# Kernel tuning notes

Hardware: AMD Instinct MI355X
Metric: run time of the kernel (lower is better)

Reference implementation:

```python
import jax, jax.numpy as jnp
import numpy as np

N = 4096
D = 512
H = 3


def setup_inputs() -> dict:
    key = jax.random.key(0)
    k1, k2, k3 = jax.random.split(key, 3)
    graph_info = (jax.random.uniform(k1, (N, N)) < 0.01).astype(jnp.float32)
    h = jax.random.normal(k2, (N, D), dtype=jnp.float32)
    # xavier_normal_ with relu gain: std = sqrt(2) * sqrt(2/(fan_in+fan_out))
    std = np.sqrt(2.0) * np.sqrt(2.0 / (D + H))
    P = jax.random.normal(k3, (D, H), dtype=jnp.float32) * jnp.float32(std)
    return {"graph_info": graph_info, "h": h, "P": P}


def reference(graph_info, h, P):
    # graph_info_1 = spmm(graph_info^T, I)^T == graph_info (identity densification)
    mask = graph_info > 0                                  # [N, N]
    E = jax.nn.relu(h @ P)                                 # [N, H] per-node scores, all heads
    NEG = jnp.float32(-9e15)
    # e is broadcast along rows: att[i, j] = E[j, k] where edge (i->j) exists
    logits = jnp.where(mask[None, :, :], E.T[:, None, :], NEG)  # [H, N, N]
    att = jax.nn.softmax(logits, axis=-1)                  # row-softmax per head
    hh = jnp.einsum('hij,jd->hid', att, h)                 # [H, N, D] aggregate
    # sum_flag == 1: scale each row i by its degree (rowsum of graph_info_1)
    rowsum = jnp.sum(graph_info, axis=-1)                  # [N]
    hh = hh * rowsum[None, :, None]
    # multi_head > 1, concat=False: sum over heads
    return jnp.sum(hh, axis=0)                             # [N, D]
```

## Files before the change

### kernel.cpp

```cpp
#include <hip/hip_runtime.h>
#include <stdint.h>

#define NN 4096
#define DD 512
#define NH 3
#define WMAX 128

typedef float        f32x4 __attribute__((ext_vector_type(4)));
typedef unsigned int u32x4 __attribute__((ext_vector_type(4)));

__device__ __forceinline__ unsigned short f2bf_rn(float x) {
    union { float f; uint32_t u; } v; v.f = x;
    uint32_t u = v.u;
    uint32_t r = (u + 0x7FFFu + ((u >> 16) & 1u)) >> 16;
    return (unsigned short)r;
}
__device__ __forceinline__ float bflo(uint32_t u) {
    union { uint32_t u; float f; } v; v.u = u << 16; return v.f;
}
__device__ __forceinline__ float bfhi(uint32_t u) {
    union { uint32_t u; float f; } v; v.u = u & 0xFFFF0000u; return v.f;
}

__global__ __launch_bounds__(256) void prep_scan_kernel(
    const float* __restrict__ g, const float* __restrict__ h,
    const float* __restrict__ P, float* __restrict__ w,
    unsigned short* __restrict__ hb, unsigned long long* __restrict__ bits)
{
    const int b = blockIdx.x;
    const int tid = threadIdx.x;
    if (b < NN) {
        const int row = b, wv = tid >> 6, ln = tid & 63;
        const f32x4* g4 = (const f32x4*)(g + (size_t)row * NN);
        f32x4 v[4];
        #pragma unroll
        for (int it = 0; it < 4; ++it)
            v[it] = __builtin_nontemporal_load(g4 + it * 256 + tid);
        #pragma unroll
        for (int it = 0; it < 4; ++it) {
            int chunk = it * 4 + wv;
            unsigned long long m0 = __ballot(v[it].x > 0.f);
            unsigned long long m1 = __ballot(v[it].y > 0.f);
            unsigned long long m2 = __ballot(v[it].z > 0.f);
            unsigned long long m3 = __ballot(v[it].w > 0.f);
            if (ln < 4) {
                unsigned long long ms = (ln == 0) ? m0 : (ln == 1) ? m1
                                       : (ln == 2) ? m2 : m3;
                bits[(size_t)row * 64 + chunk * 4 + ln] = ms;
            }
        }
        return;
    }
    int gid = (b - NN) * 256 + tid;
    int row = gid >> 6, ln = gid & 63;
    const f32x4* h4 = (const f32x4*)(h + (size_t)row * DD);
    f32x4 va = __builtin_nontemporal_load(h4 + ln * 2);
    f32x4 vb = __builtin_nontemporal_load(h4 + ln * 2 + 1);
    float e[8] = { va.x, va.y, va.z, va.w, vb.x, vb.y, vb.z, vb.w };

    u32x4 pk;
    pk.x = (uint32_t)f2bf_rn(e[0]) | ((uint32_t)f2bf_rn(e[1]) << 16);
    pk.y = (uint32_t)f2bf_rn(e[2]) | ((uint32_t)f2bf_rn(e[3]) << 16);
    pk.z = (uint32_t)f2bf_rn(e[4]) | ((uint32_t)f2bf_rn(e[5]) << 16);
    pk.w = (uint32_t)f2bf_rn(e[6]) | ((uint32_t)f2bf_rn(e[7]) << 16);
    *(u32x4*)(hb + (size_t)row * DD + ln * 8) = pk;

    int d0 = ln * 8;
    float a0 = 0.f, a1 = 0.f, a2 = 0.f;
    #pragma unroll
    for (int k = 0; k < 8; ++k) {
        float hv = e[k];
        const float* Pr = P + (size_t)(d0 + k) * NH;
        a0 = fmaf(hv, Pr[0], a0);
        a1 = fmaf(hv, Pr[1], a1);
        a2 = fmaf(hv, Pr[2], a2);
    }
    #pragma unroll
    for (int off = 32; off > 0; off >>= 1) {
        a0 += __shfl_down(a0, off);
        a1 += __shfl_down(a1, off);
        a2 += __shfl_down(a2, off);
    }
    if (ln == 0) {
        w[row * NH + 0] = expf(fmaxf(a0, 0.f));
        w[row * NH + 1] = expf(fmaxf(a1, 0.f));
        w[row * NH + 2] = expf(fmaxf(a2, 0.f));
    }
}

__global__ __launch_bounds__(256) void agg_kernel(
    const unsigned long long* __restrict__ bits,
    const unsigned short* __restrict__ hb, const float* __restrict__ w,
    float* __restrict__ out)
{
    __shared__ int s_list[4][WMAX];
    const int tid = threadIdx.x, wv = tid >> 6, ln = tid & 63;
    const int row = blockIdx.x * 4 + wv;

    unsigned long long W = bits[(size_t)row * 64 + ln];
    int cnt = __popcll(W);
    int inc = cnt;
    #pragma unroll
    for (int d = 1; d < 64; d <<= 1) {
        int n = __shfl_up(inc, d);
        if (ln >= d) inc += n;
    }
    int nnz = __shfl(inc, 63);
    int o = inc - cnt;
    int base_col = (ln >> 2) * 256 + (ln & 3);
    unsigned long long Wt = W;
    while (Wt) {
        int bp = __builtin_ctzll(Wt); Wt &= Wt - 1;
        if (o < WMAX) s_list[wv][o] = base_col + 4 * bp;
        ++o;
    }
    __syncthreads();

    float* orow = out + (size_t)row * DD + ln * 8;
    if (nnz == 0) {
        f32x4 z4 = {0.f, 0.f, 0.f, 0.f};
        *(f32x4*)(orow) = z4; *(f32x4*)(orow + 4) = z4;
        return;
    }
    int cap = nnz < WMAX ? nnz : WMAX;

    float accA[8] = {0,0,0,0,0,0,0,0};
    float accB[8] = {0,0,0,0,0,0,0,0};
    float accC[8] = {0,0,0,0,0,0,0,0};
    float z0 = 0.f, z1 = 0.f, z2 = 0.f;
    const unsigned short* hcol = hb + ln * 8;

    u32x4 r0 = {}, r1 = {};
    float wa0 = 0.f, wa1 = 0.f, wa2 = 0.f, wb0 = 0.f, wb1 = 0.f, wb2 = 0.f;
    {
        int j = s_list[wv][0];
        r0 = *(const u32x4*)(hcol + (size_t)j * DD);
        const float* wr = w + (size_t)j * NH;
        wa0 = wr[0]; wa1 = wr[1]; wa2 = wr[2];
    }
    if (cap > 1) {
        int j = s_list[wv][1];
        r1 = *(const u32x4*)(hcol + (size_t)j * DD);
        const float* wr = w + (size_t)j * NH;
        wb0 = wr[0]; wb1 = wr[1]; wb2 = wr[2];
    }
    for (int t = 0; t < cap; ++t) {
        u32x4 r = r0;
        float c0 = wa0, c1 = wa1, c2 = wa2;
        r0 = r1; wa0 = wb0; wa1 = wb1; wa2 = wb2;
        if (t + 2 < cap) {
            int j2 = s_list[wv][t + 2];
            r1 = *(const u32x4*)(hcol + (size_t)j2 * DD);
            const float* wr2 = w + (size_t)j2 * NH;
            wb0 = wr2[0]; wb1 = wr2[1]; wb2 = wr2[2];
        }
        z0 += c0; z1 += c1; z2 += c2;
        float e[8] = { bflo(r.x), bfhi(r.x), bflo(r.y), bfhi(r.y),
                       bflo(r.z), bfhi(r.z), bflo(r.w), bfhi(r.w) };
        #pragma unroll
        for (int q = 0; q < 8; ++q) {
            accA[q] = fmaf(c0, e[q], accA[q]);
            accB[q] = fmaf(c1, e[q], accB[q]);
            accC[q] = fmaf(c2, e[q], accC[q]);
        }
    }

    float rs = (float)nnz;
    float i0 = rs / z0, i1 = rs / z1, i2 = rs / z2;
    f32x4 o0, o1;
    o0.x = fmaf(accA[0], i0, fmaf(accB[0], i1, accC[0] * i2));
    o0.y = fmaf(accA[1], i0, fmaf(accB[1], i1, accC[1] * i2));
    o0.z = fmaf(accA[2], i0, fmaf(accB[2], i1, accC[2] * i2));
    o0.w = fmaf(accA[3], i0, fmaf(accB[3], i1, accC[3] * i2));
    o1.x = fmaf(accA[4], i0, fmaf(accB[4], i1, accC[4] * i2));
    o1.y = fmaf(accA[5], i0, fmaf(accB[5], i1, accC[5] * i2));
    o1.z = fmaf(accA[6], i0, fmaf(accB[6], i1, accC[6] * i2));
    o1.w = fmaf(accA[7], i0, fmaf(accB[7], i1, accC[7] * i2));
    *(f32x4*)(orow)     = o0;
    *(f32x4*)(orow + 4) = o1;
}

extern "C" void kernel_launch(void* const* d_in, const int* in_sizes, int n_in,
                              void* d_out, int out_size, void* d_ws, size_t ws_size,
                              hipStream_t stream) {
    const float* g = (const float*)d_in[0];
    const float* h = (const float*)d_in[1];
    const float* P = (const float*)d_in[2];
    float* out = (float*)d_out;

    float* w                 = (float*)d_ws;
    unsigned long long* bits = (unsigned long long*)((char*)d_ws + (64 << 10));
    unsigned short* hb       = (unsigned short*)((char*)d_ws + (64 << 10) + ((size_t)NN * 64 * 8));

    prep_scan_kernel<<<NN + (NN * 64) / 256, 256, 0, stream>>>(g, h, P, w, hb, bits);
    agg_kernel<<<NN / 4, 256, 0, stream>>>(bits, hb, w, out);
}
```

Baseline: 129.7 us.

## Fuse prep and aggregation into one cooperative kernel with grid sync

Merges the adjacency scan, bf16 conversion, score computation and aggregation into a single cooperative kernel. Each wave builds its row's neighbour list in shared memory directly via ballot/mbcnt, so the intermediate bitmask buffer and its global round trip go away. A grid-wide sync separates producing hb/w from consuming them. This removes one launch and the bits traffic, but needs all 1024 blocks co-resident, and the sync adds a barrier cost.

```diff
diff --git a/kernel.cpp b/kernel.cpp
--- a/kernel.cpp
+++ b/kernel.cpp
@@ -1,5 +1,8 @@
 #include <hip/hip_runtime.h>
+#include <hip/hip_cooperative_groups.h>
 #include <stdint.h>
+
+namespace cg = cooperative_groups;
 
 #define NN 4096
 #define DD 512
@@ -22,40 +25,17 @@
     union { uint32_t u; float f; } v; v.u = u & 0xFFFF0000u; return v.f;
 }
 
-__global__ __launch_bounds__(256) void prep_scan_kernel(
+__global__ __launch_bounds__(256, 4) void fused_att_kernel(
     const float* __restrict__ g, const float* __restrict__ h,
     const float* __restrict__ P, float* __restrict__ w,
-    unsigned short* __restrict__ hb, unsigned long long* __restrict__ bits)
+    unsigned short* __restrict__ hb, float* __restrict__ out)
 {
-    const int b = blockIdx.x;
-    const int tid = threadIdx.x;
-    if (b < NN) {
-        const int row = b, wv = tid >> 6, ln = tid & 63;
-        const f32x4* g4 = (const f32x4*)(g + (size_t)row * NN);
-        f32x4 v[4];
-        #pragma unroll
-        for (int it = 0; it < 4; ++it)
-            v[it] = __builtin_nontemporal_load(g4 + it * 256 + tid);
-        #pragma unroll
-        for (int it = 0; it < 4; ++it) {
-            int chunk = it * 4 + wv;
-            unsigned long long m0 = __ballot(v[it].x > 0.f);
-            unsigned long long m1 = __ballot(v[it].y > 0.f);
-            unsigned long long m2 = __ballot(v[it].z > 0.f);
-            unsigned long long m3 = __ballot(v[it].w > 0.f);
-            if (ln < 4) {
-                unsigned long long ms = (ln == 0) ? m0 : (ln == 1) ? m1
-                                       : (ln == 2) ? m2 : m3;
-                bits[(size_t)row * 64 + chunk * 4 + ln] = ms;
-            }
-        }
-        return;
-    }
-    int gid = (b - NN) * 256 + tid;
-    int row = gid >> 6, ln = gid & 63;
+    __shared__ int s_list[4][WMAX];
+    const int tid = threadIdx.x, wv = tid >> 6, ln = tid & 63;
+    const int row = blockIdx.x * 4 + wv;
+
     const f32x4* h4 = (const f32x4*)(h + (size_t)row * DD);
-    f32x4 va = __builtin_nontemporal_load(h4 + ln * 2);
-    f32x4 vb = __builtin_nontemporal_load(h4 + ln * 2 + 1);
+    f32x4 va = h4[ln * 2], vb = h4[ln * 2 + 1];
     float e[8] = { va.x, va.y, va.z, va.w, vb.x, vb.y, vb.z, vb.w };
 
     u32x4 pk;
@@ -65,56 +45,62 @@
     pk.w = (uint32_t)f2bf_rn(e[6]) | ((uint32_t)f2bf_rn(e[7]) << 16);
     *(u32x4*)(hb + (size_t)row * DD + ln * 8) = pk;
 
-    int d0 = ln * 8;
-    float a0 = 0.f, a1 = 0.f, a2 = 0.f;
+    {
+        int d0 = ln * 8;
+        float a0 = 0.f, a1 = 0.f, a2 = 0.f;
+        #pragma unroll
+        for (int k = 0; k < 8; ++k) {
+            float hv = e[k];
+            const float* Pr = P + (size_t)(d0 + k) * NH;
+            a0 = fmaf(hv, Pr[0], a0);
+            a1 = fmaf(hv, Pr[1], a1);
+            a2 = fmaf(hv, Pr[2], a2);
+        }
+        #pragma unroll
+        for (int off = 32; off > 0; off >>= 1) {
+            a0 += __shfl_down(a0, off);
+            a1 += __shfl_down(a1, off);
+            a2 += __shfl_down(a2, off);
+        }
+        if (ln == 0) {
+            w[row * NH + 0] = expf(fmaxf(a0, 0.f));
+            w[row * NH + 1] = expf(fmaxf(a1, 0.f));
+            w[row * NH + 2] = expf(fmaxf(a2, 0.f));
+        }
+    }
+
+    int cnt = 0;
+    const f32x4* g4 = (const f32x4*)(g + (size_t)row * NN);
     #pragma unroll
-    for (int k = 0; k < 8; ++k) {
-        float hv = e[k];
-        const float* Pr = P + (size_t)(d0 + k) * NH;
-        a0 = fmaf(hv, Pr[0], a0);
-        a1 = fmaf(hv, Pr[1], a1);
-        a2 = fmaf(hv, Pr[2], a2);
+    for (int batch = 0; batch < 2; ++batch) {
+        f32x4 v[8];
+        #pragma unroll
+        for (int k = 0; k < 8; ++k)
+            v[k] = g4[(batch * 8 + k) * 64 + ln];
+        #pragma unroll
+        for (int k = 0; k < 8; ++k) {
+            int i = batch * 8 + k;
+            float comp[4] = { v[k].x, v[k].y, v[k].z, v[k].w };
+            int col0 = 256 * i + 4 * ln;
+            #pragma unroll
+            for (int c = 0; c < 4; ++c) {
+                bool p = comp[c] > 0.f;
+                unsigned long long m = __ballot(p);
+                if (p) {
+                    unsigned pre = __builtin_amdgcn_mbcnt_lo((unsigned)m, 0u);
+                    pre = __builtin_amdgcn_mbcnt_hi((unsigned)(m >> 32), pre);
+                    int pos = cnt + (int)pre;
+                    if (pos < WMAX) s_list[wv][pos] = col0 + c;
+                }
+                cnt += __popcll(m);
+            }
+        }
     }
-    #pragma unroll
-    for (int off = 32; off > 0; off >>= 1) {
-        a0 += __shfl_down(a0, off);
-        a1 += __shfl_down(a1, off);
-        a2 += __shfl_down(a2, off);
-    }
-    if (ln == 0) {
-        w[row * NH + 0] = expf(fmaxf(a0, 0.f));
-        w[row * NH + 1] = expf(fmaxf(a1, 0.f));
-        w[row * NH + 2] = expf(fmaxf(a2, 0.f));
-    }
-}
+    int nnz = cnt;
+    int cap = nnz < WMAX ? nnz : WMAX;
 
-__global__ __launch_bounds__(256) void agg_kernel(
-    const unsigned long long* __restrict__ bits,
-    const unsigned short* __restrict__ hb, const float* __restrict__ w,
-    float* __restrict__ out)
-{
-    __shared__ int s_list[4][WMAX];
-    const int tid = threadIdx.x, wv = tid >> 6, ln = tid & 63;
-    const int row = blockIdx.x * 4 + wv;
-
-    unsigned long long W = bits[(size_t)row * 64 + ln];
-    int cnt = __popcll(W);
-    int inc = cnt;
-    #pragma unroll
-    for (int d = 1; d < 64; d <<= 1) {
-        int n = __shfl_up(inc, d);
-        if (ln >= d) inc += n;
-    }
-    int nnz = __shfl(inc, 63);
-    int o = inc - cnt;
-    int base_col = (ln >> 2) * 256 + (ln & 3);
-    unsigned long long Wt = W;
-    while (Wt) {
-        int bp = __builtin_ctzll(Wt); Wt &= Wt - 1;
-        if (o < WMAX) s_list[wv][o] = base_col + 4 * bp;
-        ++o;
-    }
-    __syncthreads();
+    __threadfence();
+    cg::this_grid().sync();
 
     float* orow = out + (size_t)row * DD + ln * 8;
     if (nnz == 0) {
@@ -122,7 +108,6 @@
         *(f32x4*)(orow) = z4; *(f32x4*)(orow + 4) = z4;
         return;
     }
-    int cap = nnz < WMAX ? nnz : WMAX;
 
     float accA[8] = {0,0,0,0,0,0,0,0};
     float accB[8] = {0,0,0,0,0,0,0,0};
@@ -155,13 +140,13 @@
             wb0 = wr2[0]; wb1 = wr2[1]; wb2 = wr2[2];
         }
         z0 += c0; z1 += c1; z2 += c2;
-        float e[8] = { bflo(r.x), bfhi(r.x), bflo(r.y), bfhi(r.y),
-                       bflo(r.z), bfhi(r.z), bflo(r.w), bfhi(r.w) };
+        float ee[8] = { bflo(r.x), bfhi(r.x), bflo(r.y), bfhi(r.y),
+                        bflo(r.z), bfhi(r.z), bflo(r.w), bfhi(r.w) };
         #pragma unroll
         for (int q = 0; q < 8; ++q) {
-            accA[q] = fmaf(c0, e[q], accA[q]);
-            accB[q] = fmaf(c1, e[q], accB[q]);
-            accC[q] = fmaf(c2, e[q], accC[q]);
+            accA[q] = fmaf(c0, ee[q], accA[q]);
+            accB[q] = fmaf(c1, ee[q], accB[q]);
+            accC[q] = fmaf(c2, ee[q], accC[q]);
         }
     }
 
@@ -188,10 +173,11 @@
     const float* P = (const float*)d_in[2];
     float* out = (float*)d_out;
 
-    float* w                 = (float*)d_ws;
-    unsigned long long* bits = (unsigned long long*)((char*)d_ws + (64 << 10));
-    unsigned short* hb       = (unsigned short*)((char*)d_ws + (64 << 10) + ((size_t)NN * 64 * 8));
+    float* w           = (float*)d_ws;
+    unsigned short* hb = (unsigned short*)((char*)d_ws + (64 << 10));
 
-    prep_scan_kernel<<<NN + (NN * 64) / 256, 256, 0, stream>>>(g, h, P, w, hb, bits);
-    agg_kernel<<<NN / 4, 256, 0, stream>>>(bits, hb, w, out);
+    void* args[] = { (void*)&g, (void*)&h, (void*)&P,
+                     (void*)&w, (void*)&hb, (void*)&out };
+    hipLaunchCooperativeKernel((const void*)fused_att_kernel,
+                               dim3(NN / 4), dim3(256), args, 0, stream);
 }
```

Measured after the change: 310.3 us. +139.2%, slower.
